# Performance work log

Hardware: AMD Instinct MI355X
Metric: run time of the kernel (lower is better)

Reference implementation:

```python
import jax, jax.numpy as jnp
import numpy as np

N_BATCH, CH, HW, KERNEL, STRIDE, VC = 8, 256, 96, 8, 3, 512


def setup_inputs() -> dict:
    key = jax.random.key(0)
    k0, k1, k2, k3 = jax.random.split(key, 4)
    kk = KERNEL * KERNEL
    x = jax.random.normal(k0, (N_BATCH, CH, HW, HW), dtype=jnp.float32)
    # 1x1 conv weight [vc, ch, 1, 1] stored as [vc, ch]
    conv_w = jax.random.normal(k1, (VC, CH), dtype=jnp.float32) * 0.05
    # integrate_mask_activation: Linear(ch+kk, 3ch) -> LeakyReLU(0.2) -> Linear(3ch, ch) -> Tanh
    W1 = jax.random.normal(k2, (3 * CH, CH + kk), dtype=jnp.float32) * 0.02
    b1 = jnp.zeros((3 * CH,), dtype=jnp.float32)
    W2 = jax.random.normal(k3, (CH, 3 * CH), dtype=jnp.float32) * 0.02
    b2 = jnp.zeros((CH,), dtype=jnp.float32)
    return {"x": x, "conv_w": conv_w, "W1": W1, "b1": b1, "W2": W2, "b2": b2}


def _unfold(x, k, s):
    # torch.nn.Unfold(kernel=(k,k), stride=s) -> patches [n, L, c, k, k]
    n, c, h, w = x.shape
    oh = (h - k) // s + 1
    ow = (w - k) // s + 1
    ih = (jnp.arange(oh) * s)[:, None] + jnp.arange(k)[None, :]  # [oh, k]
    iw = (jnp.arange(ow) * s)[:, None] + jnp.arange(k)[None, :]  # [ow, k]
    p = x[:, :, ih, :]          # [n, c, oh, k, w]
    p = p[:, :, :, :, iw]       # [n, c, oh, k, ow, k]
    p = p.transpose(0, 2, 4, 1, 3, 5)  # [n, oh, ow, c, k, k]
    return p.reshape(n, oh * ow, c, k, k), oh * ow


def reference(x, conv_w, W1, b1, W2, b2):
    k = KERNEL
    kk = k * k
    n, c, h, w = x.shape
    patches, L = _unfold(x, k, STRIDE)           # [n, L, c, k, k]
    N = n * L
    p = patches.reshape(N, c, k, k)

    # GenerateMask_2_0: normalized similarity via 1x1 conv
    x_norm = jnp.sqrt((p ** 2).sum(1))           # [N, k, k]
    w_norm = jnp.sqrt((conv_w ** 2).sum(1))      # [vc]
    y = jnp.einsum('nchw,vc->nvhw', p, conv_w)   # [N, vc, k, k]
    y = y / (x_norm[:, None, :, :] * w_norm[None, :, None, None])

    vc = conv_w.shape[0]
    y_flat = y.reshape(N, vc * kk)
    idx = jnp.argmax(y_flat, axis=1)                       # topk(k=1)
    max_sim = jnp.take_along_axis(y_flat, idx[:, None], axis=1)  # [N, 1]
    max_ch = idx // kk                                     # codebook index [N]
    col = idx % kk                                         # spatial index [N]

    rows = jnp.arange(N)
    sim_map_max = y.reshape(N, vc, kk)[rows, max_ch]       # [N, kk]
    max_act = p.reshape(N, c, kk)[rows, :, col]            # [N, c]
    vc_vec = conv_w[max_ch]                                # [N, c]
    integ = max_act * max_sim + vc_vec * (1.0 - max_sim)   # blend with codebook

    # integrate_mask_activation MLP
    inp = jnp.concatenate([integ, sim_map_max], axis=1)    # [N, c + kk]
    h1 = inp @ W1.T + b1
    h1 = jnp.where(h1 > 0, h1, 0.2 * h1)                   # LeakyReLU(0.2)
    out = jnp.tanh(h1 @ W2.T + b2)                         # [N, c]
    return out.reshape(n, L, c)
```

## Files before the change

### kernel.cpp

```cpp
#include <hip/hip_runtime.h>
#include <hip/hip_fp16.h>
#include <math.h>

#define NB 8
#define CHN 256
#define HWD 96
#define PIXN (HWD*HWD)
#define TOTPIX (NB*PIXN)
#define VCN 512
#define OHW 30
#define LPP (OHW*OHW)
#define NPATCH (NB*LPP)
#define INPD 320
#define HID 768
#define MTP 456

typedef unsigned short u16;
typedef __attribute__((ext_vector_type(8))) short bf16x8;
typedef __attribute__((ext_vector_type(8))) unsigned short us8;
typedef __attribute__((ext_vector_type(4))) float f32x4;

__device__ __forceinline__ float f4c(const float4 v, int i){
  return i==0 ? v.x : i==1 ? v.y : i==2 ? v.z : v.w;
}
__device__ __forceinline__ u16 bfrn(float f){
  unsigned u = __float_as_uint(f);
  return (u16)((u + 0x7fffu + ((u>>16)&1u)) >> 16);
}
__device__ __forceinline__ float bf2f(u16 h){
  return __uint_as_float(((unsigned)h)<<16);
}


template<int NS>
__device__ __forceinline__ void split_body(const float* __restrict__ src,
                                           u16* __restrict__ dst, int K,
                                           int rt, int kk, int kkc, int lane){
  const int qr = lane>>4, col = lane&15;
  const float* s = src + (size_t)(rt*16+col)*K + kk*32 + qr*8;
  us8 h1, h2, h3;
  #pragma unroll
  for (int j=0;j<8;j++){
    float a = s[j];
    u16 x1 = bfrn(a);  float r1 = a - bf2f(x1);
    u16 x2 = bfrn(r1); float r2 = r1 - bf2f(x2);
    h1[j]=x1; h2[j]=x2; h3[j]=bfrn(r2);
  }
  size_t base = ((size_t)(rt*kkc + kk)*NS)*512 + lane*8;
  *(us8*)&dst[base]     = h1;
  *(us8*)&dst[base+512] = h2;
  if (NS == 3) *(us8*)&dst[base+1024] = h3;
}

__global__ __launch_bounds__(64) void prep_k(
    const float* __restrict__ cw, const float* __restrict__ W1,
    const float* __restrict__ W2, u16* __restrict__ wf,
    u16* __restrict__ w1f, u16* __restrict__ w2f, float* __restrict__ invw){
  int b = blockIdx.x;
  const int lane = threadIdx.x;
  if (b < 256){ split_body<3>(cw, wf, CHN, b>>3, b&7, 8, lane); return; }
  b -= 256;
  if (b < 480){ split_body<2>(W1, w1f, INPD, b/10, b%10, 10, lane); return; }
  b -= 480;
  if (b < 384){ split_body<2>(W2, w2f, HID, b/24, b%24, 24, lane); return; }
  b -= 384;
  const float4 a = *(const float4*)&cw[(size_t)b*CHN + lane*4];
  float s = fmaf(a.x,a.x, fmaf(a.y,a.y, fmaf(a.z,a.z, a.w*a.w)));
  #pragma unroll
  for (int off=32; off; off>>=1) s += __shfl_xor(s, off);
  if (lane==0) invw[b] = 1.0f/sqrtf(s);
}

__device__ __forceinline__ void mfma6(f32x4& c, const bf16x8* A, const bf16x8* B){
  c = __builtin_amdgcn_mfma_f32_16x16x32_bf16(A[0], B[0], c, 0,0,0);
  c = __builtin_amdgcn_mfma_f32_16x16x32_bf16(A[0], B[1], c, 0,0,0);
  c = __builtin_amdgcn_mfma_f32_16x16x32_bf16(A[1], B[0], c, 0,0,0);
  c = __builtin_amdgcn_mfma_f32_16x16x32_bf16(A[0], B[2], c, 0,0,0);
  c = __builtin_amdgcn_mfma_f32_16x16x32_bf16(A[1], B[1], c, 0,0,0);
  c = __builtin_amdgcn_mfma_f32_16x16x32_bf16(A[2], B[0], c, 0,0,0);
}

__global__ __launch_bounds__(256,2) void gemm_z_k(
    const float* __restrict__ x, const u16* __restrict__ wf,
    const float* __restrict__ invw,
    float* __restrict__ pbest, int* __restrict__ pbidx,
    __half* __restrict__ zf){
  __shared__ __align__(16) u16 afr[2*8*3*512];
  __shared__ float ssq2[4][32];
  __shared__ float rv[32][4];
  __shared__ int   ri[32][4];
  const int t = threadIdx.x;
  const int wv = t>>6, lane = t&63;
  const int col = lane&15, qr = lane>>4;
  const size_t p0 = (size_t)blockIdx.x * 32;
  const int img = (int)(p0 / PIXN);
  const int pl0 = (int)(p0 % PIXN);

  {
    const int pi = t & 31, bq = t >> 5;
    const int fr = pi & 15, mt = pi >> 4;
    const float* xb = x + ((size_t)img*CHN)*PIXN + pl0 + pi;
    float s = 0.f;
    #pragma unroll
    for (int it=0; it<4; ++it){
      const int c0 = it*64 + bq*8;
      float xv[8];
      #pragma unroll
      for (int j=0;j<8;j++) xv[j] = xb[(size_t)(c0+j)*PIXN];
      us8 h1,h2,h3;
      #pragma unroll
      for (int j=0;j<8;j++){
        const float a = xv[j];
        s = fmaf(a,a,s);
        u16 x1 = bfrn(a);  float r1 = a - bf2f(x1);
        u16 x2 = bfrn(r1);
        h1[j]=x1; h2[j]=x2; h3[j]=bfrn(r1 - bf2f(x2));
      }
      const int kk = c0 >> 5, cq = (c0>>3)&3;
      u16* dstp = &afr[((mt*8+kk)*3)*512 + (cq*16+fr)*8];
      *(us8*)dstp        = h1;
      *(us8*)(dstp+512)  = h2;
      *(us8*)(dstp+1024) = h3;
    }
    s += __shfl_xor(s, 32);
    if (lane < 32) ssq2[wv][lane] = s;
  }
  __syncthreads();

  f32x4 acc[2][8];
  #pragma unroll
  for (int i=0;i<2;i++)
    #pragma unroll
    for (int j=0;j<8;j++) acc[i][j] = (f32x4){0.f,0.f,0.f,0.f};
  const size_t loff = (size_t)lane*8;
  const int loff16 = lane*8;

  bf16x8 P[4][3], Q[4][3];
  #pragma unroll
  for (int q=0;q<4;q++){
    const size_t bb = (((size_t)(wv*8+q)*8 + 0)*3)*512 + loff;
    P[q][0] = *(const bf16x8*)&wf[bb];
    P[q][1] = *(const bf16x8*)&wf[bb+512];
    P[q][2] = *(const bf16x8*)&wf[bb+1024];
  }
  for (int kk=0; kk<8; ++kk){
    bf16x8 a0[3], a1[3];
    {
      const int ab0 = (kk*3)*512 + loff16;
      const int ab1 = ((8+kk)*3)*512 + loff16;
      a0[0] = *(const bf16x8*)&afr[ab0];
      a0[1] = *(const bf16x8*)&afr[ab0+512];
      a0[2] = *(const bf16x8*)&afr[ab0+1024];
      a1[0] = *(const bf16x8*)&afr[ab1];
      a1[1] = *(const bf16x8*)&afr[ab1+512];
      a1[2] = *(const bf16x8*)&afr[ab1+1024];
    }
    #pragma unroll
    for (int q=0;q<4;q++){
      const size_t bb = (((size_t)(wv*8+4+q)*8 + kk)*3)*512 + loff;
      Q[q][0] = *(const bf16x8*)&wf[bb];
      Q[q][1] = *(const bf16x8*)&wf[bb+512];
      Q[q][2] = *(const bf16x8*)&wf[bb+1024];
    }
    #pragma unroll
    for (int q=0;q<4;q++){
      mfma6(acc[0][q], a0, P[q]);
      mfma6(acc[1][q], a1, P[q]);
    }
    if (kk < 7){
      #pragma unroll
      for (int q=0;q<4;q++){
        const size_t bb = (((size_t)(wv*8+q)*8 + (kk+1))*3)*512 + loff;
        P[q][0] = *(const bf16x8*)&wf[bb];
        P[q][1] = *(const bf16x8*)&wf[bb+512];
        P[q][2] = *(const bf16x8*)&wf[bb+1024];
      }
    }
    #pragma unroll
    for (int q=0;q<4;q++){
      mfma6(acc[0][4+q], a0, Q[q]);
      mfma6(acc[1][4+q], a1, Q[q]);
    }
  }

  float iw[8];
  #pragma unroll
  for (int ni=0;ni<8;ni++) iw[ni] = invw[wv*128 + ni*16 + col];
  #pragma unroll
  for (int mi=0;mi<2;mi++){
    #pragma unroll
    for (int r=0;r<4;r++){
      const int P2 = mi*16 + qr*4 + r;
      const float sq = ssq2[0][P2] + ssq2[1][P2] + ssq2[2][P2] + ssq2[3][P2];
      const float ip = rsqrtf(sq);
      float bz = -1e30f; int bvi = 0;
      #pragma unroll
      for (int ni=0;ni<8;ni++){
        const float z = f4c(*(const float4*)&acc[mi][ni], r) * ip * iw[ni];
        const int vv = wv*128 + ni*16 + col;
        zf[(p0+P2)*VCN + vv] = __float2half(z);
        if (z > bz){ bz = z; bvi = vv; }
      }
      #pragma unroll
      for (int off=1; off<16; off<<=1){
        const float oz = __shfl_xor(bz, off);
        const int  oi = __shfl_xor(bvi, off);
        if (oz > bz || (oz == bz && oi < bvi)){ bz = oz; bvi = oi; }
      }
      if (col == 0){ rv[P2][wv] = bz; ri[P2][wv] = bvi; }
    }
  }
  __syncthreads();
  if (t < 32){
    float best = rv[t][0]; int bi = ri[t][0];
    #pragma unroll
    for (int s=1;s<4;s++){
      float z2 = rv[t][s]; int i2 = ri[t][s];
      if (z2 > best || (z2 == best && i2 < bi)){ best = z2; bi = i2; }
    }
    pbest[p0+t] = best; pbidx[p0+t] = bi;
  }
}

__global__ __launch_bounds__(64) void select_k(
    const float* __restrict__ x, const float* __restrict__ cw,
    const __half* __restrict__ zf,
    const float* __restrict__ pbest, const int* __restrict__ pbidx,
    u16* __restrict__ inpf){
  __shared__ float wlds[256];
  __shared__ float xcol[256];
  __shared__ float simv[64];
  const int q = blockIdx.x;
  const int lane = threadIdx.x;
  const int n = q / LPP, l = q % LPP;
  const int oy = l / OHW, ox = l % OHW;
  const int pl = (oy*3 + (lane >> 3))*HWD + (ox*3 + (lane & 7));
  const int p = n*PIXN + pl;
  const int rt = q >> 4, ql = q & 15;
  float val = pbest[p];
  int flat = pbidx[p]*64 + lane;
  #pragma unroll
  for (int off=32; off>0; off>>=1){
    float ov = __shfl_xor(val, off);
    int of = __shfl_xor(flat, off);
    if (ov > val || (ov == val && of < flat)){ val = ov; flat = of; }
  }
  const int mch = flat >> 6;
  const int pos = flat & 63;
  const float ms = val;
  *(float4*)&wlds[lane*4] = *(const float4*)&cw[(size_t)mch*CHN + lane*4];
  simv[lane] = __half2float(zf[(size_t)p*VCN + mch]);
  const int wpl = (oy*3 + (pos>>3))*HWD + (ox*3 + (pos&7));
  const float* xb = x + (size_t)n*CHN*PIXN + wpl;
  #pragma unroll
  for (int j=0;j<4;j++) xcol[lane*4+j] = xb[(size_t)(lane*4+j)*PIXN];
  __syncthreads();
  if (lane < 32){
    const int kk = lane >> 2, qr = lane & 3;
    const float om = 1.0f - ms;
    const int c0 = kk*32 + qr*8;
    us8 p1, p2;
    #pragma unroll
    for (int j=0;j<8;j++){
      float v = fmaf(xcol[c0+j], ms, wlds[c0+j]*om);
      u16 s1 = bfrn(v);
      p1[j] = s1; p2[j] = bfrn(v - bf2f(s1));
    }
    const size_t ob = ((size_t)(rt*10 + kk)*2)*512 + (qr*16 + ql)*8;
    *(us8*)&inpf[ob]     = p1;
    *(us8*)&inpf[ob+512] = p2;
  }
  if (lane < 16){
    const int s = lane >> 3, kk = 8 + ((lane >> 2) & 1), qr = lane & 3;
    us8 pv;
    #pragma unroll
    for (int j=0;j<8;j++){
      float v = simv[(kk-8)*32 + qr*8 + j];
      u16 s1 = bfrn(v);
      pv[j] = (s == 0) ? s1 : bfrn(v - bf2f(s1));
    }
    const size_t ob = ((size_t)(rt*10 + kk)*2 + s)*512 + (qr*16 + ql)*8;
    *(us8*)&inpf[ob] = pv;
  }
}

__global__ __launch_bounds__(256,2) void mlp1_k(
    const u16* __restrict__ af, const u16* __restrict__ bf,
    const float* __restrict__ bias, u16* __restrict__ h1f){
  const int kkc = INPD >> 5;
  const int t = threadIdx.x;
  const int n0 = blockIdx.x*128, m0 = blockIdx.y*128;
  const int lane = t&63, wv = t>>6;
  const int mq = wv&1, nq = wv>>1;
  const int col = lane&15, qr = lane>>4;
  const size_t loff = (size_t)lane*8;
  const int ptA0 = (m0>>4) + mq*4;
  const int ntB0 = (n0>>4) + nq*4;
  f32x4 acc[4][4];
  #pragma unroll
  for (int i=0;i<4;i++)
    #pragma unroll
    for (int j=0;j<4;j++) acc[i][j] = (f32x4){0.f,0.f,0.f,0.f};

  for (int kk=0; kk<kkc; kk++){
    bf16x8 a[4][2];
    #pragma unroll
    for (int mi=0;mi<4;mi++){
      const size_t ab = (((size_t)(ptA0+mi)*kkc + kk)*2)*512 + loff;
      a[mi][0] = *(const bf16x8*)&af[ab];
      a[mi][1] = *(const bf16x8*)&af[ab+512];
    }
    #pragma unroll
    for (int ni=0;ni<4;ni++){
      const size_t bb = (((size_t)(ntB0+ni)*kkc + kk)*2)*512 + loff;
      const bf16x8 b1 = *(const bf16x8*)&bf[bb];
      const bf16x8 b2 = *(const bf16x8*)&bf[bb+512];
      #pragma unroll
      for (int mi=0;mi<4;mi++){
        f32x4 c = acc[mi][ni];
        c = __builtin_amdgcn_mfma_f32_16x16x32_bf16(a[mi][0], b1, c, 0,0,0);
        c = __builtin_amdgcn_mfma_f32_16x16x32_bf16(a[mi][0], b2, c, 0,0,0);
        c = __builtin_amdgcn_mfma_f32_16x16x32_bf16(a[mi][1], b1, c, 0,0,0);
        acc[mi][ni] = c;
      }
    }
  }
  float bb4[4];
  #pragma unroll
  for (int ni=0;ni<4;ni++) bb4[ni] = bias[n0 + nq*64 + ni*16 + col];
  #pragma unroll
  for (int mi=0;mi<4;mi++){
    const int rt2 = (m0>>4) + mq*4 + mi;
    #pragma unroll
    for (int r=0;r<4;r++){
      #pragma unroll
      for (int ni=0;ni<4;ni++){
        float v = f4c(*(const float4*)&acc[mi][ni], r) + bb4[ni];
        v = v > 0.f ? v : 0.2f*v;
        u16 s1 = bfrn(v);
        u16 s2 = bfrn(v - bf2f(s1));
        const int kk2 = (n0>>5) + nq*2 + (ni>>1);
        const int qn = (ni&1)*2 + (col>>3);
        const size_t ob = ((size_t)(rt2*24 + kk2)*2)*512 + (qn*16 + qr*4 + r)*8 + (col&7);
        h1f[ob] = s1; h1f[ob+512] = s2;
      }
    }
  }
}

__global__ __launch_bounds__(256,2) void mlp2_k(
    const u16* __restrict__ af, const u16* __restrict__ bf,
    const float* __restrict__ bias, float* __restrict__ C){
  const int kkc = HID >> 5;
  const int t = threadIdx.x;
  const int n0 = blockIdx.x*128, m0 = blockIdx.y*128;
  const int lane = t&63, wv = t>>6;
  const int mq = wv&1, nq = wv>>1;
  const int col = lane&15, qr = lane>>4;
  const size_t loff = (size_t)lane*8;
  const int ptA0 = (m0>>4) + mq*4;
  const int ntB0 = (n0>>4) + nq*4;
  f32x4 acc[4][4];
  #pragma unroll
  for (int i=0;i<4;i++)
    #pragma unroll
    for (int j=0;j<4;j++) acc[i][j] = (f32x4){0.f,0.f,0.f,0.f};

  for (int kk=0; kk<kkc; kk++){
    bf16x8 a[4][2];
    #pragma unroll
    for (int mi=0;mi<4;mi++){
      const size_t ab = (((size_t)(ptA0+mi)*kkc + kk)*2)*512 + loff;
      a[mi][0] = *(const bf16x8*)&af[ab];
      a[mi][1] = *(const bf16x8*)&af[ab+512];
    }
    #pragma unroll
    for (int ni=0;ni<4;ni++){
      const size_t bb = (((size_t)(ntB0+ni)*kkc + kk)*2)*512 + loff;
      const bf16x8 b1 = *(const bf16x8*)&bf[bb];
      const bf16x8 b2 = *(const bf16x8*)&bf[bb+512];
      #pragma unroll
      for (int mi=0;mi<4;mi++){
        f32x4 c = acc[mi][ni];
        c = __builtin_amdgcn_mfma_f32_16x16x32_bf16(a[mi][0], b1, c, 0,0,0);
        c = __builtin_amdgcn_mfma_f32_16x16x32_bf16(a[mi][0], b2, c, 0,0,0);
        c = __builtin_amdgcn_mfma_f32_16x16x32_bf16(a[mi][1], b1, c, 0,0,0);
        acc[mi][ni] = c;
      }
    }
  }
  float bb4[4];
  #pragma unroll
  for (int ni=0;ni<4;ni++) bb4[ni] = bias[n0 + nq*64 + ni*16 + col];
  #pragma unroll
  for (int mi=0;mi<4;mi++){
    #pragma unroll
    for (int r=0;r<4;r++){
      const int row = m0 + mq*64 + mi*16 + qr*4 + r;
      if (row < NPATCH){
        #pragma unroll
        for (int ni=0;ni<4;ni++){
          float v = f4c(*(const float4*)&acc[mi][ni], r) + bb4[ni];
          C[(size_t)row*CHN + n0 + nq*64 + ni*16 + col] = tanhf(v);
        }
      }
    }
  }
}

extern "C" void kernel_launch(void* const* d_in, const int* in_sizes, int n_in,
                              void* d_out, int out_size, void* d_ws, size_t ws_size,
                              hipStream_t stream){
  const float* x  = (const float*)d_in[0];
  const float* cw = (const float*)d_in[1];
  const float* W1 = (const float*)d_in[2];
  const float* b1 = (const float*)d_in[3];
  const float* W2 = (const float*)d_in[4];
  const float* b2 = (const float*)d_in[5];
  float* out = (float*)d_out;
  float* ws = (float*)d_ws;
  float* invw  = ws;
  float* pbest = invw + VCN;
  int*   pbidx = (int*)(pbest + TOTPIX);
  u16*   wf    = (u16*)(pbidx + TOTPIX);
  u16*   w1f   = wf + (size_t)32*8*3*512;
  u16*   w2f   = w1f + (size_t)48*10*2*512;
  u16*   inpf  = w2f + (size_t)16*24*2*512;
  __half* zf   = (__half*)(inpf + (size_t)MTP*10*2*512);
  u16*   h1f   = (u16*)zf;

  prep_k<<<1632,64,0,stream>>>(cw, W1, W2, wf, w1f, w2f, invw);
  gemm_z_k<<<TOTPIX/32,256,0,stream>>>(x, wf, invw, pbest, pbidx, zf);
  select_k<<<NPATCH,64,0,stream>>>(x, cw, zf, pbest, pbidx, inpf);
  mlp1_k<<<dim3(HID/128, (NPATCH+127)/128),256,0,stream>>>(inpf, w1f, b1, h1f);
  mlp2_k<<<dim3(CHN/128, (NPATCH+127)/128),256,0,stream>>>(h1f, w2f, b2, out);
}
```

Before: 367.9 us.

## Drop B-fragment register prefetch, raise occupancy to 3 blocks, add MFMA priority

Removes the software-pipelined P/Q double-buffer of codebook weight fragments and loads each group of four B fragments just before use. This frees VGPRs so the launch bound can be raised from 2 to 3 blocks per CU. Each MFMA burst is also wrapped in s_setprio to favour matrix issue. The trade is more latency hiding through extra waves instead of explicit prefetch, with the risk of exposed global-load latency or spills under the tighter register budget.

```diff
diff --git a/kernel.cpp b/kernel.cpp
--- a/kernel.cpp
+++ b/kernel.cpp
@@ -80,7 +80,7 @@
   c = __builtin_amdgcn_mfma_f32_16x16x32_bf16(A[2], B[0], c, 0,0,0);
 }
 
-__global__ __launch_bounds__(256,2) void gemm_z_k(
+__global__ __launch_bounds__(256,3) void gemm_z_k(
     const float* __restrict__ x, const u16* __restrict__ wf,
     const float* __restrict__ invw,
     float* __restrict__ pbest, int* __restrict__ pbidx,
@@ -134,15 +134,6 @@
     for (int j=0;j<8;j++) acc[i][j] = (f32x4){0.f,0.f,0.f,0.f};
   const size_t loff = (size_t)lane*8;
   const int loff16 = lane*8;
-
-  bf16x8 P[4][3], Q[4][3];
-  #pragma unroll
-  for (int q=0;q<4;q++){
-    const size_t bb = (((size_t)(wv*8+q)*8 + 0)*3)*512 + loff;
-    P[q][0] = *(const bf16x8*)&wf[bb];
-    P[q][1] = *(const bf16x8*)&wf[bb+512];
-    P[q][2] = *(const bf16x8*)&wf[bb+1024];
-  }
   for (int kk=0; kk<8; ++kk){
     bf16x8 a0[3], a1[3];
     {
@@ -156,30 +147,24 @@
       a1[2] = *(const bf16x8*)&afr[ab1+1024];
     }
     #pragma unroll
-    for (int q=0;q<4;q++){
-      const size_t bb = (((size_t)(wv*8+4+q)*8 + kk)*3)*512 + loff;
-      Q[q][0] = *(const bf16x8*)&wf[bb];
-      Q[q][1] = *(const bf16x8*)&wf[bb+512];
-      Q[q][2] = *(const bf16x8*)&wf[bb+1024];
-    }
-    #pragma unroll
-    for (int q=0;q<4;q++){
-      mfma6(acc[0][q], a0, P[q]);
-      mfma6(acc[1][q], a1, P[q]);
-    }
-    if (kk < 7){
+    for (int h=0; h<2; ++h){
+      bf16x8 bg[4][3];
       #pragma unroll
       for (int q=0;q<4;q++){
-        const size_t bb = (((size_t)(wv*8+q)*8 + (kk+1))*3)*512 + loff;
-        P[q][0] = *(const bf16x8*)&wf[bb];
-        P[q][1] = *(const bf16x8*)&wf[bb+512];
-        P[q][2] = *(const bf16x8*)&wf[bb+1024];
-      }
-    }
-    #pragma unroll
-    for (int q=0;q<4;q++){
-      mfma6(acc[0][4+q], a0, Q[q]);
-      mfma6(acc[1][4+q], a1, Q[q]);
+        const int ni = h*4+q;
+        const size_t bb = (((size_t)(wv*8+ni)*8 + kk)*3)*512 + loff;
+        bg[q][0] = *(const bf16x8*)&wf[bb];
+        bg[q][1] = *(const bf16x8*)&wf[bb+512];
+        bg[q][2] = *(const bf16x8*)&wf[bb+1024];
+      }
+      __builtin_amdgcn_s_setprio(1);
+      #pragma unroll
+      for (int q=0;q<4;q++){
+        const int ni = h*4+q;
+        mfma6(acc[0][ni], a0, bg[q]);
+        mfma6(acc[1][ni], a1, bg[q]);
+      }
+      __builtin_amdgcn_s_setprio(0);
     }
   }
 
```

Result: faster. 318.9 us (-13.3%).
